# Performance work log

Hardware: AMD Instinct MI355X
Metric: run time of the kernel (lower is better)

## Reference

```python
import jax, jax.numpy as jnp
import numpy as np

DIM = 512
LENTH = 256
B, N1, N2 = 16, 2048, 2048


def setup_inputs() -> dict:
    key = jax.random.key(0)
    k1, k2, kq, kk, kv, kbq, kbk, kbv = jax.random.split(key, 8)
    s_q = 1.0 / np.sqrt(DIM)
    s_kv = 1.0 / np.sqrt(LENTH)
    return {
        "input1": jax.random.normal(k1, (B, N1, DIM), jnp.float32),
        "input2": jax.random.normal(k2, (B, N2, LENTH), jnp.float32),
        "Wq": jax.random.uniform(kq, (DIM, DIM), jnp.float32, -s_q, s_q),
        "bq": jax.random.uniform(kbq, (DIM,), jnp.float32, -s_q, s_q),
        "Wk": jax.random.uniform(kk, (LENTH, DIM), jnp.float32, -s_kv, s_kv),
        "bk": jax.random.uniform(kbk, (DIM,), jnp.float32, -s_kv, s_kv),
        "Wv": jax.random.uniform(kv, (LENTH, DIM), jnp.float32, -s_kv, s_kv),
        "bv": jax.random.uniform(kbv, (DIM,), jnp.float32, -s_kv, s_kv),
    }


def reference(input1, input2, Wq, bq, Wk, bk, Wv, bv):
    scale = jnp.asarray(DIM ** 0.5, input1.dtype)
    q = input1 @ Wq + bq                      # [B, N1, D]
    k = input2 @ Wk + bk                      # [B, N2, D]
    v = input2 @ Wv + bv                      # [B, N2, D]
    scores = jnp.einsum('bqd,bkd->bqk', q, k) / scale  # [B, N1, N2]
    attn = jax.nn.softmax(scores, axis=-1)
    return jnp.einsum('bqk,bkd->bqd', attn, v)  # [B, N1, D]
```

## Files before the change

kernel.cpp:

```cpp
#include <hip/hip_runtime.h>


#define DIMD 512
#define LENL 256
#define BATCH 16
#define NQ 2048
#define NKV 2048

using bf16x8 = __attribute__((ext_vector_type(8))) __bf16;
using f32x4  = __attribute__((ext_vector_type(4))) float;
typedef unsigned short u16;

__device__ __forceinline__ u16 f2bf(float f) {
  union { float f; unsigned u; } x; x.f = f;
  return (u16)((x.u + 0x7fffu + ((x.u >> 16) & 1u)) >> 16);
}
__device__ __forceinline__ float bf2f(u16 b) {
  union { unsigned u; float f; } x; x.u = ((unsigned)b) << 16;
  return x.f;
}

__global__ __launch_bounds__(256) void k_cvt(const float* __restrict__ src,
                                             u16* __restrict__ dst, int n4) {
  int i = blockIdx.x * blockDim.x + threadIdx.x;
  int stride = gridDim.x * blockDim.x;
  for (; i < n4; i += stride) {
    float4 v = ((const float4*)src)[i];
    ushort4 o;
    o.x = f2bf(v.x); o.y = f2bf(v.y); o.z = f2bf(v.z); o.w = f2bf(v.w);
    ((ushort4*)dst)[i] = o;
  }
}

__global__ __launch_bounds__(256) void k_transpose(const float* __restrict__ W,
                                                   u16* __restrict__ WT,
                                                   int K, int N) {
  __shared__ float t[32][33];
  int bx = blockIdx.x * 32;
  int by = blockIdx.y * 32;
  int tx = threadIdx.x, ty = threadIdx.y;
#pragma unroll
  for (int i = 0; i < 4; i++)
    t[ty + 8 * i][tx] = W[(size_t)(by + ty + 8 * i) * N + (bx + tx)];
  __syncthreads();
#pragma unroll
  for (int i = 0; i < 4; i++)
    WT[(size_t)(bx + ty + 8 * i) * K + (by + tx)] = f2bf(t[tx][ty + 8 * i]);
}

__global__ __launch_bounds__(256) void k_cvt_t(const float* __restrict__ in2,
                                               u16* __restrict__ A2,
                                               u16* __restrict__ TX2) {
  __shared__ u16 t[32][33];
  int bx = blockIdx.x * 32;
  int by = blockIdx.y * 32;
  long z = blockIdx.z;
  const float* s = in2 + z * (2048L * 256);
  u16* a = A2 + z * (2048L * 256);
  u16* d = TX2 + z * (256L * 2048);
  int tx = threadIdx.x, ty = threadIdx.y;
#pragma unroll
  for (int i = 0; i < 4; i++) {
    u16 v = f2bf(s[(size_t)(by + ty + 8 * i) * 256 + (bx + tx)]);
    a[(size_t)(by + ty + 8 * i) * 256 + (bx + tx)] = v;
    t[ty + 8 * i][tx] = v;
  }
  __syncthreads();
#pragma unroll
  for (int i = 0; i < 4; i++)
    d[(size_t)(bx + ty + 8 * i) * 2048 + (by + tx)] = t[tx][ty + 8 * i];
}

__global__ __launch_bounds__(256) void k_bqp(const float* __restrict__ bq,
                                             const float* __restrict__ Wk,
                                             float* __restrict__ bqp) {
  int n = threadIdx.x;
  float s = 0.f;
  for (int o = 0; o < 512; o += 4) {
    float4 w = *(const float4*)&Wk[(size_t)n * 512 + o];
    float4 b = *(const float4*)&bq[o];
    s += w.x * b.x + w.y * b.y + w.z * b.z + w.w * b.w;
  }
  bqp[n] = s;
}

__device__ __forceinline__ void gl_lds16(const void* g, void* l) {
  __builtin_amdgcn_global_load_lds(
      (const __attribute__((address_space(1))) void*)g,
      (__attribute__((address_space(3))) void*)l, 16, 0, 0);
}

__device__ __forceinline__ void xcd_swz(int& bx, int& by, int& bz) {
  const int nx = gridDim.x, ny = gridDim.y, nz = gridDim.z;
  const long nwg = (long)nx * ny * nz;
  if (nwg & 7) return;
  long lin = (long)bx + (long)nx * ((long)by + (long)ny * bz);
  const long q = nwg >> 3;
  const long nl = (lin & 7) * q + (lin >> 3);
  bx = (int)(nl % nx);
  long r2 = nl / nx;
  by = (int)(r2 % ny);
  bz = (int)(r2 / ny);
}

#define MF(a, b, c) __builtin_amdgcn_mfma_f32_16x16x32_bf16(a, b, c, 0, 0, 0)

__global__ __launch_bounds__(512, 2) void k_fused_su(
    const u16* __restrict__ Qp, const u16* __restrict__ X2g,
    const u16* __restrict__ TXg, u16* __restrict__ U,
    float* __restrict__ Iv, float scale) {
  __shared__ __align__(16) char lds[139776];
  float* part = (float*)(lds + 139264);

  int bxi = blockIdx.x, byi = blockIdx.y, bzi = blockIdx.z;
  xcd_swz(bxi, byi, bzi);
  const int tid = threadIdx.x, lane = tid & 63, wid = tid >> 6;
  const int fr = lane & 15, kq = lane >> 4;
  const int fr7 = fr & 7, fr3 = fr & 3;
  const int row0 = bxi * 128;
  const long z = byi;
  const int kh = wid & 1, rq = wid >> 1;
  const int wr = wid >> 2, wc = wid & 3;

  if (tid < 128) part[tid] = 0.f;

  bf16x8 qf[2][8];
  {
    const u16* qb = Qp + ((long)z * 2048 + row0 + rq * 32) * 256;
#pragma unroll
    for (int ni = 0; ni < 2; ni++)
#pragma unroll
      for (int kk = 0; kk < 8; kk++)
        qf[ni][kk] =
            *(const bf16x8*)(qb + (ni * 16 + fr) * 256 + kk * 32 + kq * 8);
  }

  const u16* gX2 = X2g + (long)z * (2048 * 256);
  const u16* gTX = TXg + (long)z * (256 * 2048);
  const int xrow = tid >> 5, xs = tid & 31;
  const int trow = tid >> 2, ts = tid & 3;

#define STG(ii, b) { \
  _Pragma("unroll") for (int p = 0; p < 2; p++) { \
    const int r_ = p * 16 + xrow; \
    gl_lds16(gX2 + ((long)(ii) * 32 + r_) * 256 + (xs ^ (r_ & 7)) * 8, \
             lds + (b) * 16384 + (p * 512 + tid) * 16); } \
  _Pragma("unroll") for (int p = 0; p < 2; p++) { \
    const int r_ = p * 128 + trow; \
    gl_lds16(gTX + (long)r_ * 2048 + (ii) * 32 + (ts ^ (r_ & 3)) * 8, \
             lds + 65536 + (b) * 16384 + (p * 512 + tid) * 16); } }

  f32x4 accU[4][4];
  const f32x4 zero = {0.f, 0.f, 0.f, 0.f};
#pragma unroll
  for (int m = 0; m < 4; m++)
#pragma unroll
    for (int n = 0; n < 4; n++) accU[m][n] = zero;
  float rs0 = 0.f, rs1 = 0.f;

  STG(0, 0);
  STG(1, 1);

  for (int i = 0; i < 64; i++) {
    const int cur = i & 3;
    const int pre = (i + 2 > 63) ? 63 : i + 2;
    STG(pre, (i + 2) & 3);
    asm volatile("s_waitcnt vmcnt(8)" ::: "memory");
    __builtin_amdgcn_sched_barrier(0);
    __builtin_amdgcn_s_barrier();
    __builtin_amdgcn_sched_barrier(0);

    f32x4 accS[2];
    accS[0] = zero; accS[1] = zero;
    const char* xb = lds + cur * 16384;
    __builtin_amdgcn_s_setprio(1);
#pragma unroll
    for (int kk = 0; kk < 8; kk++) {
      bf16x8 xf = *(const bf16x8*)(xb + (kh * 16 + fr) * 512 +
                                   (((kk * 4 + kq) ^ fr7) << 4));
      accS[0] = MF(xf, qf[0][kk], accS[0]);
      accS[1] = MF(xf, qf[1][kk], accS[1]);
    }
    __builtin_amdgcn_s_setprio(0);

#pragma unroll
    for (int ni = 0; ni < 2; ni++) {
      u16 e[4];
      float sum4 = 0.f;
#pragma unroll
      for (int r = 0; r < 4; r++) {
        float v = accS[ni][r] * scale;
        float ef = __expf(fminf(v, 30.f));
        e[r] = f2bf(ef);
        sum4 += bf2f(e[r]);
      }
      if (ni == 0) rs0 += sum4; else rs1 += sum4;
      unsigned long long w =
          (unsigned long long)((unsigned)e[0] | ((unsigned)e[1] << 16)) |
          ((unsigned long long)((unsigned)e[2] | ((unsigned)e[3] << 16)) << 32);
      const int row = rq * 32 + ni * 16 + fr;
      const int slot16 = (kh * 2 + (kq >> 1)) ^ fr3;
      *(unsigned long long*)(lds + 131072 + row * 64 + (slot16 << 4) +
                             (kq & 1) * 8) = w;
    }
    asm volatile("s_waitcnt lgkmcnt(0)" ::: "memory");
    __builtin_amdgcn_sched_barrier(0);
    __builtin_amdgcn_s_barrier();
    __builtin_amdgcn_sched_barrier(0);

    const char* tb = lds + 65536 + cur * 16384;
    __builtin_amdgcn_s_setprio(1);
    {
      bf16x8 sf[4], tf[4];
#pragma unroll
      for (int m = 0; m < 4; m++)
        sf[m] = *(const bf16x8*)(lds + 131072 + (wr * 64 + m * 16 + fr) * 64 +
                                 ((kq ^ fr3) << 4));
#pragma unroll
      for (int n = 0; n < 4; n++)
        tf[n] = *(const bf16x8*)(tb + (wc * 64 + n * 16 + fr) * 64 +
                                 ((kq ^ fr3) << 4));
#pragma unroll
      for (int m = 0; m < 4; m++)
#pragma unroll
        for (int n = 0; n < 4; n++)
          accU[m][n] = MF(sf[m], tf[n], accU[m][n]);
    }
    __builtin_amdgcn_s_setprio(0);
  }
#undef STG

  {
    float s0 = rs0, s1 = rs1;
    s0 += __shfl_xor(s0, 16); s0 += __shfl_xor(s0, 32);
    s1 += __shfl_xor(s1, 16); s1 += __shfl_xor(s1, 32);
    if (lane < 16) {
      atomicAdd(&part[rq * 32 + lane], s0);
      atomicAdd(&part[rq * 32 + 16 + lane], s1);
    }
  }
  __syncthreads();
  if (tid < 128) Iv[z * 2048 + row0 + tid] = 1.f / part[tid];

  u16* ub = U + ((long)z * 2048 + row0) * 256;
#pragma unroll
  for (int m = 0; m < 4; m++)
#pragma unroll
    for (int n = 0; n < 4; n++) {
      const int col = wc * 64 + n * 16 + fr;
#pragma unroll
      for (int r = 0; r < 4; r++) {
        const int row = wr * 64 + m * 16 + kq * 4 + r;
        ub[row * 256 + col] = f2bf(accU[m][n][r]);
      }
    }
}

#define SA(p, h, l, T) \
  gl_lds16(gA + (long)((h) * 128 + (l) * 64) * lda + (T) * 64, \
           dA + (p) * 32768 + (h) * 16384 + (l) * 8192)
#define SB(p, h, l, T) \
  gl_lds16(gB + (long)((h) * 128 + (l) * 64) * ldb + (T) * 64, \
           dB + (p) * (BNH * 16384) + (h) * 16384 + (l) * 8192)
#define RD_A(p, mh) { _Pragma("unroll") for (int m = 0; m < 4; m++) { \
    afr[m][0] = *(const bf16x8*)(lds + (p) * 32768 + aoffb + ((mh) * 64 + m * 16) * 128 + sb0); \
    afr[m][1] = *(const bf16x8*)(lds + (p) * 32768 + aoffb + ((mh) * 64 + m * 16) * 128 + sb1); } }
#define RD_B(p, nh, BF) { _Pragma("unroll") for (int n = 0; n < 2; n++) { \
    BF[n][0] = *(const bf16x8*)(lds + (p) * (BNH * 16384) + boffb + (((nh) * 2 + n) * 16) * 128 + sb0); \
    BF[n][1] = *(const bf16x8*)(lds + (p) * (BNH * 16384) + boffb + (((nh) * 2 + n) * 16) * 128 + sb1); } }
#define MFMA_QUAD(mh, nh, BF) { \
  _Pragma("unroll") for (int m = 0; m < 4; m++) \
  _Pragma("unroll") for (int n = 0; n < 2; n++) \
  _Pragma("unroll") for (int kk = 0; kk < 2; kk++) \
    acc[(mh) * 4 + m][(nh) * 2 + n] = MF(afr[m][kk], BF[n][kk], \
                                         acc[(mh) * 4 + m][(nh) * 2 + n]); }
#define BAR_MFMA_OPEN() \
  __builtin_amdgcn_sched_barrier(0); \
  __builtin_amdgcn_s_barrier(); \
  asm volatile("s_waitcnt lgkmcnt(0)" ::: "memory"); \
  __builtin_amdgcn_sched_barrier(0); \
  __builtin_amdgcn_s_setprio(1)
#define PH_CLOSE() \
  __builtin_amdgcn_s_setprio(0); \
  __builtin_amdgcn_sched_barrier(0); \
  __builtin_amdgcn_s_barrier(); \
  __builtin_amdgcn_sched_barrier(0)
#define PH_CLOSE_VM(N) \
  __builtin_amdgcn_s_setprio(0); \
  asm volatile("s_waitcnt vmcnt(" #N ")" ::: "memory"); \
  __builtin_amdgcn_sched_barrier(0); \
  __builtin_amdgcn_s_barrier(); \
  __builtin_amdgcn_sched_barrier(0)

template <int BNH, int OUT_BF16, int BIAS_MODE, int FUSE>
__global__ __launch_bounds__(512, 2) void k_gemm256(
    const u16* __restrict__ A, const u16* __restrict__ BT,
    void* __restrict__ Cv, const float* __restrict__ bias,
    const float* __restrict__ finv,
    int K, int lda, int ldb, int ldc, long sA, long sB, long sC, float scale) {
  __shared__ __align__(16) char lds[65536 + BNH * 32768 + 1024];
  float* part = (float*)(lds + 65536 + BNH * 32768);

  int bxi = blockIdx.x, byi = blockIdx.y, bzi = blockIdx.z;
  xcd_swz(bxi, byi, bzi);
  const int tid = threadIdx.x, lane = tid & 63, wid = tid >> 6;
  const int wr = wid >> 2, wc = wid & 3;
  const int fr = lane & 15, kq = lane >> 4, fr7 = fr & 7;
  const int brow = byi * 256, bcol = bxi * (BNH * 128);
  const long z = bzi;

  if (FUSE == 3 && tid < 256) part[tid] = finv[z * 2048 + brow + tid];

  const int srow = tid >> 3;
  const int sslot = (tid & 7) ^ (srow & 7);
  const u16* gA = A + z * sA + (long)(brow + srow) * lda + sslot * 8;
  const u16* gB = BT + z * sB + (long)(bcol + srow) * ldb + sslot * 8;
  char* dA = lds + tid * 16;
  char* dB = lds + 65536 + tid * 16;

  const int aoffb = (wr * 128 + fr) * 128;
  const int boffb = 65536 + (wc * (BNH * 32) + fr) * 128;
  const int sb0 = (kq ^ fr7) * 16;
  const int sb1 = ((4 + kq) ^ fr7) * 16;

  f32x4 acc[8][2 * BNH];
  const f32x4 zero = {0.f, 0.f, 0.f, 0.f};
#pragma unroll
  for (int m = 0; m < 8; m++)
#pragma unroll
    for (int n = 0; n < 2 * BNH; n++) acc[m][n] = zero;

  bf16x8 afr[4][2], bf0[2][2], bf1[2][2];
  const int iters = K >> 7;

  if (BNH == 2) {
    SA(0, 0, 0, 0); SA(0, 0, 1, 0); SA(0, 1, 0, 0); SA(0, 1, 1, 0);
    SB(0, 0, 0, 0); SB(0, 0, 1, 0); SB(0, 1, 0, 0); SB(0, 1, 1, 0);
    SB(1, 0, 0, 1); SB(1, 0, 1, 1); SB(1, 1, 0, 1); SB(1, 1, 1, 1);
    asm volatile("s_waitcnt vmcnt(4)" ::: "memory");
    __builtin_amdgcn_sched_barrier(0);
    __builtin_amdgcn_s_barrier();
    for (int i = 0; i < iters; i++) {
      const int t1 = 2 * i + 1, p0 = 2 * i + 2, p1 = 2 * i + 3;
      const bool more = (i + 1 < iters);
      RD_A(0, 0); RD_B(0, 0, bf0);
      SA(1, 0, 0, t1); SA(1, 0, 1, t1);
      BAR_MFMA_OPEN(); MFMA_QUAD(0, 0, bf0); PH_CLOSE();
      RD_B(0, 1, bf1);
      SA(1, 1, 0, t1); SA(1, 1, 1, t1);
      BAR_MFMA_OPEN(); MFMA_QUAD(0, 1, bf1); PH_CLOSE();
      RD_A(0, 1);
      if (more) { SB(0, 0, 0, p0); SB(0, 0, 1, p0); }
      BAR_MFMA_OPEN(); MFMA_QUAD(1, 0, bf0); PH_CLOSE();
      if (more) { SB(0, 1, 0, p0); SB(0, 1, 1, p0); }
      BAR_MFMA_OPEN(); MFMA_QUAD(1, 1, bf1);
      if (more) { PH_CLOSE_VM(4); } else { PH_CLOSE_VM(0); }
      RD_A(1, 0); RD_B(1, 0, bf0);
      if (more) { SA(0, 0, 0, p0); SA(0, 0, 1, p0); }
      BAR_MFMA_OPEN(); MFMA_QUAD(0, 0, bf0); PH_CLOSE();
      RD_B(1, 1, bf1);
      if (more) { SA(0, 1, 0, p0); SA(0, 1, 1, p0); }
      BAR_MFMA_OPEN(); MFMA_QUAD(0, 1, bf1); PH_CLOSE();
      RD_A(1, 1);
      if (more) { SB(1, 0, 0, p1); SB(1, 0, 1, p1); }
      BAR_MFMA_OPEN(); MFMA_QUAD(1, 0, bf0); PH_CLOSE();
      if (more) { SB(1, 1, 0, p1); SB(1, 1, 1, p1); }
      BAR_MFMA_OPEN(); MFMA_QUAD(1, 1, bf1);
      if (more) { PH_CLOSE_VM(4); } else { PH_CLOSE_VM(0); }
    }
  } else {
    SA(0, 0, 0, 0); SA(0, 0, 1, 0); SA(0, 1, 0, 0); SA(0, 1, 1, 0);
    SB(0, 0, 0, 0); SB(0, 0, 1, 0);
    SB(1, 0, 0, 1); SB(1, 0, 1, 1);
    asm volatile("s_waitcnt vmcnt(2)" ::: "memory");
    __builtin_amdgcn_sched_barrier(0);
    __builtin_amdgcn_s_barrier();
    for (int i = 0; i < iters; i++) {
      const int t1 = 2 * i + 1, p0 = 2 * i + 2, p1 = 2 * i + 3;
      const bool more = (i + 1 < iters);
      RD_A(0, 0); RD_B(0, 0, bf0);
      SA(1, 0, 0, t1); SA(1, 0, 1, t1);
      BAR_MFMA_OPEN(); MFMA_QUAD(0, 0, bf0); PH_CLOSE();
      RD_A(0, 1);
      SA(1, 1, 0, t1); SA(1, 1, 1, t1);
      if (more) { SB(0, 0, 0, p0); SB(0, 0, 1, p0); }
      BAR_MFMA_OPEN(); MFMA_QUAD(1, 0, bf0);
      if (more) { PH_CLOSE_VM(2); } else { PH_CLOSE_VM(0); }
      RD_A(1, 0); RD_B(1, 0, bf1);
      if (more) { SA(0, 0, 0, p0); SA(0, 0, 1, p0); }
      BAR_MFMA_OPEN(); MFMA_QUAD(0, 0, bf1); PH_CLOSE();
      RD_A(1, 1);
      if (more) { SA(0, 1, 0, p0); SA(0, 1, 1, p0);
                  SB(1, 0, 0, p1); SB(1, 0, 1, p1); }
      BAR_MFMA_OPEN(); MFMA_QUAD(1, 0, bf1);
      if (more) { PH_CLOSE_VM(2); } else { PH_CLOSE_VM(0); }
    }
  }

  const long zC = z * sC;
#pragma unroll
  for (int mi = 0; mi < 8; mi++) {
    const int r0 = brow + wr * 128 + mi * 16 + kq * 4;
#pragma unroll
    for (int n = 0; n < 2 * BNH; n++) {
      const int c = bcol + wc * (BNH * 32) + n * 16 + fr;
#pragma unroll
      for (int r = 0; r < 4; r++) {
        float v = acc[mi][n][r] * scale;
        if (BIAS_MODE == 1) v += bias[c];
        if (BIAS_MODE == 2) v += bias[r0 + r];
        if (FUSE == 3) v = v * part[r0 + r - brow] + bias[c];
        const long off = zC + (long)(r0 + r) * ldc + c;
        if (OUT_BF16) ((u16*)Cv)[off] = f2bf(v);
        else          ((float*)Cv)[off] = v;
      }
    }
  }
}

extern "C" void kernel_launch(void* const* d_in, const int* in_sizes, int n_in,
                              void* d_out, int out_size, void* d_ws, size_t ws_size,
                              hipStream_t stream) {
  (void)in_sizes; (void)n_in; (void)out_size;
  const float* in1 = (const float*)d_in[0];
  const float* in2 = (const float*)d_in[1];
  const float* Wq  = (const float*)d_in[2];
  const float* bq  = (const float*)d_in[3];
  const float* Wk  = (const float*)d_in[4];
  const float* Wv  = (const float*)d_in[6];
  const float* bv  = (const float*)d_in[7];
  float* out = (float*)d_out;

  const size_t MB = 1024ull * 1024ull;
  if (ws_size < 100 * MB) return;

  char* ws = (char*)d_ws;
  u16* A1   = (u16*)(ws + 0);
  u16* A2   = (u16*)(ws + 32 * MB);
  u16* Qp   = (u16*)(ws + 48 * MB);
  u16* TX2  = (u16*)(ws + 64 * MB);
  u16* U    = (u16*)(ws + 80 * MB);
  u16* Wqb  = (u16*)(ws + 96 * MB);
  u16* Wkb  = (u16*)(ws + 96 * MB + 524288);
  u16* WvT  = (u16*)(ws + 96 * MB + 786432);
  u16* WT1  = (u16*)(ws + 97 * MB);
  float* bqp = (float*)(ws + 97 * MB + 262144);
  float* Iv  = (float*)(ws + 97 * MB + 524288);

  k_cvt<<<2048, 256, 0, stream>>>(in1, A1, 32768 * 512 / 4);
  k_cvt<<<256, 256, 0, stream>>>(Wq, Wqb, 512 * 512 / 4);
  k_cvt<<<128, 256, 0, stream>>>(Wk, Wkb, 256 * 512 / 4);
  k_cvt_t<<<dim3(8, 64, 16), dim3(32, 8), 0, stream>>>(in2, A2, TX2);
  k_transpose<<<dim3(16, 8), dim3(32, 8), 0, stream>>>(Wv, WvT, LENL, DIMD);
  k_gemm256<2, 1, 0, 0><<<dim3(2, 1, 1), 512, 0, stream>>>(
      Wkb, Wqb, WT1, nullptr, nullptr, 512, 512, 512, 512, 0, 0, 0, 1.f);
  k_bqp<<<1, 256, 0, stream>>>(bq, Wk, bqp);
  k_gemm256<1, 1, 1, 0><<<dim3(2, 128, 1), 512, 0, stream>>>(
      A1, WT1, Qp, bqp, nullptr, 512, 512, 512, 256, 0, 0, 0, 1.f);
  const float qk_scale = 0.044194173824159216f;
  k_fused_su<<<dim3(16, 16), 512, 0, stream>>>(Qp, A2, TX2, U, Iv, qk_scale);
  k_gemm256<2, 0, 0, 3><<<dim3(2, 128, 1), 512, 0, stream>>>(
      U, WvT, out, bv, Iv, 256, 256, 256, 512, 0, 0, 0, 1.f);
}
```

Measured before the change: 188.7 us.

## Software-pipeline QK and PV stages with 64-key tiles and double-buffered scores

Doubles the key tile from 32 to 64 rows, halving loop iterations and barriers. The score tile gets two LDS buffers, so the QK^T/exp stage for tile i runs in the same barrier phase as the PV accumulation for tile i-1. This removes one barrier per iteration and lets the two MFMA phases interleave. The cost is a larger LDS footprint (160 KB), which may limit occupancy, plus a more complex prologue and epilogue; the row-sum scratch is now zeroed after the loop.

```diff
diff --git a/kernel.cpp b/kernel.cpp
--- a/kernel.cpp
+++ b/kernel.cpp
@@ -109,21 +109,18 @@
     const u16* __restrict__ Qp, const u16* __restrict__ X2g,
     const u16* __restrict__ TXg, u16* __restrict__ U,
     float* __restrict__ Iv, float scale) {
-  __shared__ __align__(16) char lds[139776];
-  float* part = (float*)(lds + 139264);
+  __shared__ __align__(16) char lds[163840];
+  float* part = (float*)(lds + 131072);
 
   int bxi = blockIdx.x, byi = blockIdx.y, bzi = blockIdx.z;
   xcd_swz(bxi, byi, bzi);
   const int tid = threadIdx.x, lane = tid & 63, wid = tid >> 6;
-  const int fr = lane & 15, kq = lane >> 4;
-  const int fr7 = fr & 7, fr3 = fr & 3;
+  const int fr = lane & 15, kq = lane >> 4, fr7 = fr & 7;
   const int row0 = bxi * 128;
   const long z = byi;
   const int kh = wid & 1, rq = wid >> 1;
   const int wr = wid >> 2, wc = wid & 3;
 
-  if (tid < 128) part[tid] = 0.f;
-
   bf16x8 qf[2][8];
   {
     const u16* qb = Qp + ((long)z * 2048 + row0 + rq * 32) * 256;
@@ -138,17 +135,63 @@
   const u16* gX2 = X2g + (long)z * (2048 * 256);
   const u16* gTX = TXg + (long)z * (256 * 2048);
   const int xrow = tid >> 5, xs = tid & 31;
-  const int trow = tid >> 2, ts = tid & 3;
-
-#define STG(ii, b) { \
-  _Pragma("unroll") for (int p = 0; p < 2; p++) { \
+  const int trow = tid >> 3, ts = tid & 7;
+
+#define STG_X2(ii, b) { \
+  _Pragma("unroll") for (int p = 0; p < 4; p++) { \
     const int r_ = p * 16 + xrow; \
-    gl_lds16(gX2 + ((long)(ii) * 32 + r_) * 256 + (xs ^ (r_ & 7)) * 8, \
-             lds + (b) * 16384 + (p * 512 + tid) * 16); } \
-  _Pragma("unroll") for (int p = 0; p < 2; p++) { \
-    const int r_ = p * 128 + trow; \
-    gl_lds16(gTX + (long)r_ * 2048 + (ii) * 32 + (ts ^ (r_ & 3)) * 8, \
-             lds + 65536 + (b) * 16384 + (p * 512 + tid) * 16); } }
+    gl_lds16(gX2 + ((long)(ii) * 64 + r_) * 256 + (xs ^ (r_ & 7)) * 8, \
+             lds + (b) * 32768 + (p * 512 + tid) * 16); } }
+#define STG_TX(ii, b) { \
+  _Pragma("unroll") for (int p = 0; p < 4; p++) { \
+    const int r_ = p * 64 + trow; \
+    gl_lds16(gTX + (long)r_ * 2048 + (ii) * 64 + (ts ^ (r_ & 7)) * 8, \
+             lds + 65536 + (b) * 32768 + (p * 512 + tid) * 16); } }
+
+#define QK_BODY(xbuf, sbuf) { \
+  f32x4 accS[2][2]; \
+  accS[0][0] = zero; accS[0][1] = zero; accS[1][0] = zero; accS[1][1] = zero; \
+  const char* xb = lds + (xbuf) * 32768; \
+  _Pragma("unroll") for (int kk = 0; kk < 8; kk++) { \
+    const int so = ((kk * 4 + kq) ^ fr7) << 4; \
+    bf16x8 xf0 = *(const bf16x8*)(xb + (kh * 32 + fr) * 512 + so); \
+    bf16x8 xf1 = *(const bf16x8*)(xb + (kh * 32 + 16 + fr) * 512 + so); \
+    accS[0][0] = MF(xf0, qf[0][kk], accS[0][0]); \
+    accS[0][1] = MF(xf0, qf[1][kk], accS[0][1]); \
+    accS[1][0] = MF(xf1, qf[0][kk], accS[1][0]); \
+    accS[1][1] = MF(xf1, qf[1][kk], accS[1][1]); \
+  } \
+  _Pragma("unroll") for (int mi = 0; mi < 2; mi++) \
+  _Pragma("unroll") for (int ni = 0; ni < 2; ni++) { \
+    u16 e[4]; float sum4 = 0.f; \
+    _Pragma("unroll") for (int r = 0; r < 4; r++) { \
+      float v = accS[mi][ni][r] * scale; \
+      float ef = __expf(fminf(v, 30.f)); \
+      e[r] = f2bf(ef); sum4 += bf2f(e[r]); \
+    } \
+    if (ni == 0) rs0 += sum4; else rs1 += sum4; \
+    unsigned long long w = \
+        (unsigned long long)((unsigned)e[0] | ((unsigned)e[1] << 16)) | \
+        ((unsigned long long)((unsigned)e[2] | ((unsigned)e[3] << 16)) << 32); \
+    const int row = rq * 32 + ni * 16 + fr; \
+    const int inrow = (kh * 64 + mi * 32 + kq * 8) ^ (fr7 << 4); \
+    *(unsigned long long*)(lds + 131072 + (sbuf) * 16384 + row * 128 + inrow) = w; \
+  } }
+
+#define PV_BODY(tbuf, sbuf) { \
+  const char* tb = lds + 65536 + (tbuf) * 32768; \
+  const char* sbase = lds + 131072 + (sbuf) * 16384; \
+  _Pragma("unroll") for (int kk = 0; kk < 2; kk++) { \
+    const int so = ((kk * 4 + kq) ^ fr7) << 4; \
+    bf16x8 sf[4], tf[4]; \
+    _Pragma("unroll") for (int m = 0; m < 4; m++) \
+      sf[m] = *(const bf16x8*)(sbase + (wr * 64 + m * 16 + fr) * 128 + so); \
+    _Pragma("unroll") for (int n = 0; n < 4; n++) \
+      tf[n] = *(const bf16x8*)(tb + (wc * 64 + n * 16 + fr) * 128 + so); \
+    _Pragma("unroll") for (int m = 0; m < 4; m++) \
+    _Pragma("unroll") for (int n = 0; n < 4; n++) \
+      accU[m][n] = MF(sf[m], tf[n], accU[m][n]); \
+  } }
 
   f32x4 accU[4][4];
   const f32x4 zero = {0.f, 0.f, 0.f, 0.f};
@@ -158,78 +201,52 @@
     for (int n = 0; n < 4; n++) accU[m][n] = zero;
   float rs0 = 0.f, rs1 = 0.f;
 
-  STG(0, 0);
-  STG(1, 1);
-
-  for (int i = 0; i < 64; i++) {
-    const int cur = i & 3;
-    const int pre = (i + 2 > 63) ? 63 : i + 2;
-    STG(pre, (i + 2) & 3);
+  STG_X2(0, 0); STG_X2(1, 1); STG_TX(0, 0);
+  asm volatile("s_waitcnt vmcnt(8)" ::: "memory");
+  __builtin_amdgcn_sched_barrier(0);
+  __builtin_amdgcn_s_barrier();
+  __builtin_amdgcn_s_setprio(1);
+  QK_BODY(0, 0);
+  __builtin_amdgcn_s_setprio(0);
+  asm volatile("s_waitcnt lgkmcnt(0)" ::: "memory");
+  __builtin_amdgcn_sched_barrier(0);
+  __builtin_amdgcn_s_barrier();
+  __builtin_amdgcn_sched_barrier(0);
+
+  for (int i = 1; i < 32; i++) {
+    const int cur = i & 1, prv = cur ^ 1;
+    const int pre = (i + 1 > 31) ? 31 : i + 1;
+    STG_X2(pre, (i + 1) & 1);
+    STG_TX(i, cur);
     asm volatile("s_waitcnt vmcnt(8)" ::: "memory");
     __builtin_amdgcn_sched_barrier(0);
     __builtin_amdgcn_s_barrier();
     __builtin_amdgcn_sched_barrier(0);
-
-    f32x4 accS[2];
-    accS[0] = zero; accS[1] = zero;
-    const char* xb = lds + cur * 16384;
     __builtin_amdgcn_s_setprio(1);
-#pragma unroll
-    for (int kk = 0; kk < 8; kk++) {
-      bf16x8 xf = *(const bf16x8*)(xb + (kh * 16 + fr) * 512 +
-                                   (((kk * 4 + kq) ^ fr7) << 4));
-      accS[0] = MF(xf, qf[0][kk], accS[0]);
-      accS[1] = MF(xf, qf[1][kk], accS[1]);
-    }
+    QK_BODY(cur, cur);
+    PV_BODY(prv, prv);
     __builtin_amdgcn_s_setprio(0);
-
-#pragma unroll
-    for (int ni = 0; ni < 2; ni++) {
-      u16 e[4];
-      float sum4 = 0.f;
-#pragma unroll
-      for (int r = 0; r < 4; r++) {
-        float v = accS[ni][r] * scale;
-        float ef = __expf(fminf(v, 30.f));
-        e[r] = f2bf(ef);
-        sum4 += bf2f(e[r]);
-      }
-      if (ni == 0) rs0 += sum4; else rs1 += sum4;
-      unsigned long long w =
-          (unsigned long long)((unsigned)e[0] | ((unsigned)e[1] << 16)) |
-          ((unsigned long long)((unsigned)e[2] | ((unsigned)e[3] << 16)) << 32);
-      const int row = rq * 32 + ni * 16 + fr;
-      const int slot16 = (kh * 2 + (kq >> 1)) ^ fr3;
-      *(unsigned long long*)(lds + 131072 + row * 64 + (slot16 << 4) +
-                             (kq & 1) * 8) = w;
-    }
     asm volatile("s_waitcnt lgkmcnt(0)" ::: "memory");
     __builtin_amdgcn_sched_barrier(0);
     __builtin_amdgcn_s_barrier();
     __builtin_amdgcn_sched_barrier(0);
-
-    const char* tb = lds + 65536 + cur * 16384;
-    __builtin_amdgcn_s_setprio(1);
-    {
-      bf16x8 sf[4], tf[4];
-#pragma unroll
-      for (int m = 0; m < 4; m++)
-        sf[m] = *(const bf16x8*)(lds + 131072 + (wr * 64 + m * 16 + fr) * 64 +
-                                 ((kq ^ fr3) << 4));
-#pragma unroll
-      for (int n = 0; n < 4; n++)
-        tf[n] = *(const bf16x8*)(tb + (wc * 64 + n * 16 + fr) * 64 +
-                                 ((kq ^ fr3) << 4));
-#pragma unroll
-      for (int m = 0; m < 4; m++)
-#pragma unroll
-        for (int n = 0; n < 4; n++)
-          accU[m][n] = MF(sf[m], tf[n], accU[m][n]);
-    }
-    __builtin_amdgcn_s_setprio(0);
-  }
-#undef STG
-
+  }
+
+  asm volatile("s_waitcnt vmcnt(0)" ::: "memory");
+  __builtin_amdgcn_sched_barrier(0);
+  __builtin_amdgcn_s_barrier();
+  __builtin_amdgcn_s_setprio(1);
+  PV_BODY(1, 1);
+  __builtin_amdgcn_s_setprio(0);
+
+#undef STG_X2
+#undef STG_TX
+#undef QK_BODY
+#undef PV_BODY
+
+  __syncthreads();
+  if (tid < 128) part[tid] = 0.f;
+  __syncthreads();
   {
     float s0 = rs0, s1 = rs1;
     s0 += __shfl_xor(s0, 16); s0 += __shfl_xor(s0, 32);
```

After: 185.3 us (median of 2 runs). No clear change (-1.8%).
